# Performance work log

Measured on AMD Instinct MI355X. Metric: run time of the kernel, lower is better.

The kernel has to match this reference:

```python
import jax, jax.numpy as jnp
import numpy as np

D_MODEL = 1024
N_HEADS = 16
HEAD_DIM = D_MODEL // N_HEADS
SEQ_LEN = 2048
BATCH = 4


def setup_inputs() -> dict:
    key = jax.random.key(0)
    k1, k2, k3 = jax.random.split(key, 3)
    x = jax.random.normal(k1, (BATCH, SEQ_LEN, D_MODEL), dtype=jnp.float32)
    # Linear weights stored as [in, out] so y = x @ W (equivalent to torch x @ W.T)
    w_qkv = jax.random.normal(k2, (D_MODEL, 3 * D_MODEL), dtype=jnp.float32) * (D_MODEL ** -0.5)
    w_proj = jax.random.normal(k3, (D_MODEL, D_MODEL), dtype=jnp.float32) * (D_MODEL ** -0.5)
    return {"x": x, "w_qkv": w_qkv, "w_proj": w_proj}


def reference(x, w_qkv, w_proj):
    B, T, C = x.shape
    qkv = x @ w_qkv  # [B, T, 3C]
    q, k, v = jnp.split(qkv, 3, axis=-1)
    # [B, H, T, hd]
    q = q.reshape(B, T, N_HEADS, HEAD_DIM).transpose(0, 2, 1, 3)
    k = k.reshape(B, T, N_HEADS, HEAD_DIM).transpose(0, 2, 1, 3)
    v = v.reshape(B, T, N_HEADS, HEAD_DIM).transpose(0, 2, 1, 3)
    scale = HEAD_DIM ** -0.5
    attn = jnp.einsum("bhqd,bhkd->bhqk", q, k) * scale  # [B, H, T, T]
    causal = jnp.tril(jnp.ones((T, T), dtype=bool))
    attn = jnp.where(causal, attn, -jnp.inf)
    attn = jax.nn.softmax(attn, axis=-1)
    out = jnp.einsum("bhqk,bhkd->bhqd", attn, v)  # [B, H, T, hd]
    out = out.transpose(0, 2, 1, 3).reshape(B, T, C)
    return out @ w_proj
```

## Files before the change

### kernel.cpp

```cpp
#include <hip/hip_runtime.h>
#include <stdint.h>


typedef __bf16 bf16x8 __attribute__((ext_vector_type(8)));
typedef float f32x4 __attribute__((ext_vector_type(4)));
typedef unsigned short u16x8 __attribute__((ext_vector_type(8)));

#define DEVINL static __device__ __forceinline__

DEVINL unsigned short f2b(float f) {
  __bf16 h = (__bf16)f;
  return __builtin_bit_cast(unsigned short, h);
}

DEVINL void gld16(const void* g, void* l) {
  __builtin_amdgcn_global_load_lds(
      (const __attribute__((address_space(1))) void*)g,
      (__attribute__((address_space(3))) void*)l, 16, 0, 0);
}

DEVINL f32x4 mfma16(bf16x8 a, bf16x8 b, f32x4 c) {
  return __builtin_amdgcn_mfma_f32_16x16x32_bf16(a, b, c, 0, 0, 0);
}

#define SCHED_FENCE() __builtin_amdgcn_sched_barrier(0)

__global__ __launch_bounds__(256) void k_cast_bf16(const float* __restrict__ in,
                                                   unsigned short* __restrict__ out,
                                                   int n8) {
  int i = blockIdx.x * 256 + threadIdx.x;
  if (i >= n8) return;
  const float4* p = (const float4*)in + (size_t)i * 2;
  float4 a = p[0], b = p[1];
  u16x8 o;
  o[0] = f2b(a.x); o[1] = f2b(a.y); o[2] = f2b(a.z); o[3] = f2b(a.w);
  o[4] = f2b(b.x); o[5] = f2b(b.y); o[6] = f2b(b.z); o[7] = f2b(b.w);
  *(u16x8*)(out + (size_t)i * 8) = o;
}

__global__ __launch_bounds__(256) void k_transpose_w(const float* __restrict__ in,
                                                     unsigned short* __restrict__ out,
                                                     int R, int C) {
  __shared__ float t[64][65];
  int ci = blockIdx.x * 64, ri = blockIdx.y * 64;
  int tid = threadIdx.x;
#pragma unroll
  for (int j = 0; j < 4; ++j) {
    int c = tid + j * 256;
    int row = c >> 4;
    int col = (c & 15) * 4;
    float4 v = *(const float4*)(in + (size_t)(ri + row) * C + ci + col);
    t[row][col] = v.x; t[row][col + 1] = v.y; t[row][col + 2] = v.z; t[row][col + 3] = v.w;
  }
  __syncthreads();
  int cc = tid >> 2;
  int seg = (tid & 3) * 16;
  u16x8 o0, o1;
#pragma unroll
  for (int j = 0; j < 8; ++j) o0[j] = f2b(t[seg + j][cc]);
#pragma unroll
  for (int j = 0; j < 8; ++j) o1[j] = f2b(t[seg + 8 + j][cc]);
  unsigned short* dst = out + (size_t)(ci + cc) * R + ri + seg;
  *(u16x8*)dst = o0;
  *(u16x8*)(dst + 8) = o1;
}

template <int MODE>
__global__ __launch_bounds__(256) void k_gemm(const unsigned short* __restrict__ A,
                                              const unsigned short* __restrict__ Bt,
                                              int M, int N, int K,
                                              float* __restrict__ Cf,
                                              unsigned short* __restrict__ qo,
                                              unsigned short* __restrict__ ko,
                                              unsigned short* __restrict__ vo,
                                              float qscale) {
  __shared__ unsigned short As[3][128 * 32];
  __shared__ unsigned short Bs[3][128 * 32];
  int tid = threadIdx.x;
  int w = tid >> 6, lane = tid & 63, l15 = lane & 15, l4 = lane >> 4;
  int nwg = gridDim.x;
  int gx = N >> 7;
  int lin = blockIdx.x;
  int nx = nwg >> 3, rr = nwg & 7;
  int xcd = lin & 7, idx = lin >> 3;
  int wgid = (xcd < rr ? xcd * (nx + 1) : rr * (nx + 1) + (xcd - rr) * nx) + idx;
  int bn = wgid % gx, bm = wgid / gx;
  int wr = (w >> 1) * 64, wc = (w & 1) * 64;
  f32x4 acc[4][4];
#pragma unroll
  for (int i = 0; i < 4; ++i)
#pragma unroll
    for (int j = 0; j < 4; ++j) acc[i][j] = (f32x4){0.f, 0.f, 0.f, 0.f};
  const char* Ab = (const char*)(A + (size_t)bm * 128 * K);
  const char* Bb = (const char*)(Bt + (size_t)bn * 128 * K);
  int Lb0 = tid * 16, Lb1 = (tid + 256) * 16;
  int Nb0 = Lb0 ^ (((Lb0 >> 7) & 3) << 4);
  int Nb1 = Lb1 ^ (((Lb1 >> 7) & 3) << 4);
  int rA0 = Nb0 >> 6, o0 = Nb0 & 63;
  int rA1 = Nb1 >> 6, o1 = Nb1 & 63;

  auto stage = [&](int kt, int buf) {
    gld16(Ab + ((size_t)rA0 * K + kt) * 2 + o0, (char*)As[buf] + Lb0);
    gld16(Bb + ((size_t)rA0 * K + kt) * 2 + o0, (char*)Bs[buf] + Lb0);
    gld16(Ab + ((size_t)rA1 * K + kt) * 2 + o1, (char*)As[buf] + Lb1);
    gld16(Bb + ((size_t)rA1 * K + kt) * 2 + o1, (char*)Bs[buf] + Lb1);
  };

  const int nkt = K >> 5;
  stage(0, 0);
  stage(32, 1);
  SCHED_FENCE();
  for (int t = 0; t < nkt; ++t) {
    int cur = t - (t / 3) * 3;
    if (t) {
      SCHED_FENCE();
      __builtin_amdgcn_s_barrier();
      SCHED_FENCE();
    }
    if (t + 2 < nkt) {
      int nb = (t + 2) - ((t + 2) / 3) * 3;
      stage((t + 2) * 32, nb);
      SCHED_FENCE();
      asm volatile("s_waitcnt vmcnt(8)" ::: "memory");
    } else if (t + 1 < nkt) {
      SCHED_FENCE();
      asm volatile("s_waitcnt vmcnt(4)" ::: "memory");
    } else {
      SCHED_FENCE();
      asm volatile("s_waitcnt vmcnt(0)" ::: "memory");
    }
    SCHED_FENCE();
    __builtin_amdgcn_s_barrier();
    SCHED_FENCE();
    const char* Ac = (const char*)As[cur];
    const char* Bc = (const char*)Bs[cur];
    bf16x8 af[4], bfr[4];
#pragma unroll
    for (int m = 0; m < 4; ++m) {
      int nat = (wr + m * 16 + l15) * 64 + l4 * 16;
      af[m] = *(const bf16x8*)(Ac + (nat ^ (((nat >> 7) & 3) << 4)));
    }
#pragma unroll
    for (int n = 0; n < 4; ++n) {
      int nat = (wc + n * 16 + l15) * 64 + l4 * 16;
      bfr[n] = *(const bf16x8*)(Bc + (nat ^ (((nat >> 7) & 3) << 4)));
    }
    __builtin_amdgcn_s_setprio(1);
#pragma unroll
    for (int m = 0; m < 4; ++m)
#pragma unroll
      for (int n = 0; n < 4; ++n)
        acc[m][n] = mfma16(af[m], bfr[n], acc[m][n]);
    __builtin_amdgcn_s_setprio(0);
  }
#pragma unroll
  for (int m = 0; m < 4; ++m) {
    int grow0 = bm * 128 + wr + m * 16 + l4 * 4;
#pragma unroll
    for (int n = 0; n < 4; ++n) {
      int gcol = bn * 128 + wc + n * 16 + l15;
      if (MODE == 1) {
#pragma unroll
        for (int r = 0; r < 4; ++r)
          Cf[(size_t)(grow0 + r) * N + gcol] = acc[m][n][r];
      } else {
        int which = gcol >> 10, rem = gcol & 1023;
        int h = rem >> 6, d = rem & 63;
        int b = grow0 >> 11, t0 = grow0 & 2047;
        if (which == 2) {
          uint32_t lo = (uint32_t)f2b(acc[m][n][0]) | ((uint32_t)f2b(acc[m][n][1]) << 16);
          uint32_t hi = (uint32_t)f2b(acc[m][n][2]) | ((uint32_t)f2b(acc[m][n][3]) << 16);
          size_t off = (((size_t)(b * 16 + h)) * 64 + d) * 2048 + t0;
          *(uint2*)(vo + off) = make_uint2(lo, hi);
        } else {
          size_t off = (((size_t)(b * 16 + h)) * 2048 + t0) * 64 + d;
#pragma unroll
          for (int r = 0; r < 4; ++r) {
            float val = acc[m][n][r];
            if (which == 0) qo[off + (size_t)r * 64] = f2b(val * qscale);
            else            ko[off + (size_t)r * 64] = f2b(val);
          }
        }
      }
    }
  }
}

__global__ __launch_bounds__(512) void k_attn(const unsigned short* __restrict__ Q,
                                              const unsigned short* __restrict__ Kt,
                                              const unsigned short* __restrict__ Vt,
                                              unsigned short* __restrict__ AO) {
  __shared__ unsigned short Ks[2][4096];
  __shared__ unsigned short Vs[2][4096];
  __shared__ unsigned short Ps[8192];
  int tid = threadIdx.x;
  int w = tid >> 6, lane = tid & 63, l15 = lane & 15, l4 = lane >> 4;
  int lin = blockIdx.x;
  int xcd = lin & 7, jj = lin >> 3;
  int bh = xcd * 8 + (jj & 7);
  int p = jj >> 3;
  const char* Kb = (const char*)(Kt + (size_t)bh * 2048 * 64);
  const char* Vb = (const char*)(Vt + (size_t)bh * 64 * 2048);
  const int swp = (l15 & 7) << 4;
  char* Pw = (char*)Ps + w * 2048;
  int b = bh >> 4, h = bh & 15;

  int Lb0 = tid * 16;
  int Nb0 = Lb0 ^ (((Lb0 >> 7) & 7) << 4);
  int d0 = Nb0 >> 7, in0 = Nb0 & 127;

  auto stage = [&](int t, int buf) {
    size_t kv0 = (size_t)t * 64;
    gld16(Kb + kv0 * 128 + Nb0, (char*)Ks[buf] + Lb0);
    gld16(Vb + (size_t)d0 * 4096 + kv0 * 2 + in0, (char*)Vs[buf] + Lb0);
  };

  auto run = [&](int qi) {
    int q0 = qi * 128;
    const unsigned short* Qb = Q + ((size_t)bh * 2048 + q0 + w * 16) * 64;
    bf16x8 qf0 = *(const bf16x8*)((const char*)Qb + l15 * 128 + l4 * 16);
    bf16x8 qf1 = *(const bf16x8*)((const char*)Qb + l15 * 128 + 64 + l4 * 16);
    f32x4 o[4];
#pragma unroll
    for (int i = 0; i < 4; ++i) o[i] = (f32x4){0.f, 0.f, 0.f, 0.f};
    float mrow = -1e30f, lrow = 0.f;
    const int ntiles = 2 * qi + 2;
    const int qgmin = q0 + w * 16;
    const int qg = qgmin + l15;
    SCHED_FENCE();
    __builtin_amdgcn_s_barrier();
    SCHED_FENCE();
    stage(0, 0);
    SCHED_FENCE();
    for (int it = 0; it < ntiles; ++it) {
      int cur = it & 1;
      if (it) {
        SCHED_FENCE();
        __builtin_amdgcn_s_barrier();
        SCHED_FENCE();
      }
      if (it + 1 < ntiles) {
        stage(it + 1, cur ^ 1);
        SCHED_FENCE();
        asm volatile("s_waitcnt vmcnt(2)" ::: "memory");
      } else {
        SCHED_FENCE();
        asm volatile("s_waitcnt vmcnt(0)" ::: "memory");
      }
      SCHED_FENCE();
      __builtin_amdgcn_s_barrier();
      SCHED_FENCE();
      if (it * 64 <= qgmin + 15) {
        const char* Kc = (const char*)Ks[cur];
        const char* Vc = (const char*)Vs[cur];
        f32x4 s[4];
        __builtin_amdgcn_s_setprio(1);
#pragma unroll
        for (int c = 0; c < 4; ++c) {
          int row = c * 16 + l15;
          int base = row * 128 + l4 * 16;
          int sw = (row & 7) << 4;
          bf16x8 k0 = *(const bf16x8*)(Kc + (base ^ sw));
          bf16x8 k1 = *(const bf16x8*)(Kc + ((base + 64) ^ sw));
          f32x4 t = mfma16(k0, qf0, (f32x4){0.f, 0.f, 0.f, 0.f});
          s[c] = mfma16(k1, qf1, t);
        }
        __builtin_amdgcn_s_setprio(0);
        if (it * 64 + 63 > qgmin) {
#pragma unroll
          for (int c = 0; c < 4; ++c) {
            int kvb = it * 64 + c * 16 + l4 * 4;
#pragma unroll
            for (int r = 0; r < 4; ++r)
              if (kvb + r > qg) s[c][r] = -1e30f;
          }
        }
        float mx = fmaxf(fmaxf(fmaxf(s[0][0], s[0][1]), fmaxf(s[0][2], s[0][3])),
                         fmaxf(fmaxf(s[1][0], s[1][1]), fmaxf(s[1][2], s[1][3])));
        mx = fmaxf(mx, fmaxf(fmaxf(fmaxf(s[2][0], s[2][1]), fmaxf(s[2][2], s[2][3])),
                             fmaxf(fmaxf(s[3][0], s[3][1]), fmaxf(s[3][2], s[3][3]))));
        mx = fmaxf(mx, __shfl_xor(mx, 16));
        mx = fmaxf(mx, __shfl_xor(mx, 32));
        float mn = fmaxf(mrow, mx);
        float corr = __builtin_amdgcn_exp2f(mrow - mn);
        mrow = mn;
        float rs = 0.f;
#pragma unroll
        for (int c = 0; c < 4; ++c) {
          float p0 = __builtin_amdgcn_exp2f(s[c][0] - mn);
          float p1 = __builtin_amdgcn_exp2f(s[c][1] - mn);
          float p2 = __builtin_amdgcn_exp2f(s[c][2] - mn);
          float p3 = __builtin_amdgcn_exp2f(s[c][3] - mn);
          rs += (p0 + p1) + (p2 + p3);
          uint32_t lo = (uint32_t)f2b(p0) | ((uint32_t)f2b(p1) << 16);
          uint32_t hi = (uint32_t)f2b(p2) | ((uint32_t)f2b(p3) << 16);
          *(uint2*)(Pw + ((l15 * 128 + c * 32 + l4 * 8) ^ swp)) = make_uint2(lo, hi);
        }
        rs += __shfl_xor(rs, 16);
        rs += __shfl_xor(rs, 32);
        lrow = lrow * corr + rs;
        float corr_r[4];
#pragma unroll
        for (int r = 0; r < 4; ++r) corr_r[r] = __shfl(corr, l4 * 4 + r);
#pragma unroll
        for (int dc = 0; dc < 4; ++dc)
#pragma unroll
          for (int r = 0; r < 4; ++r) o[dc][r] *= corr_r[r];
        bf16x8 pa[2];
#pragma unroll
        for (int kc = 0; kc < 2; ++kc)
          pa[kc] = *(const bf16x8*)(Pw + ((l15 * 128 + kc * 64 + l4 * 16) ^ swp));
        __builtin_amdgcn_s_setprio(1);
#pragma unroll
        for (int dc = 0; dc < 4; ++dc) {
#pragma unroll
          for (int kc = 0; kc < 2; ++kc) {
            int vrow = dc * 16 + l15;
            int vnat = vrow * 128 + kc * 64 + l4 * 16;
            bf16x8 vb = *(const bf16x8*)(Vc + (vnat ^ ((vrow & 7) << 4)));
            o[dc] = mfma16(pa[kc], vb, o[dc]);
          }
        }
        __builtin_amdgcn_s_setprio(0);
      }
    }
    float inv[4];
#pragma unroll
    for (int r = 0; r < 4; ++r) inv[r] = 1.f / __shfl(lrow, l4 * 4 + r);
#pragma unroll
    for (int dc = 0; dc < 4; ++dc) {
#pragma unroll
      for (int r = 0; r < 4; ++r) {
        int t = q0 + w * 16 + l4 * 4 + r;
        AO[((size_t)(b * 2048 + t)) * 1024 + h * 64 + dc * 16 + l15] =
            f2b(o[dc][r] * inv[r]);
      }
    }
  };

  run(15 - p);
  run(p);
}

extern "C" void kernel_launch(void* const* d_in, const int* in_sizes, int n_in,
                              void* d_out, int out_size, void* d_ws, size_t ws_size,
                              hipStream_t stream) {
  const float* x      = (const float*)d_in[0];
  const float* w_qkv  = (const float*)d_in[1];
  const float* w_proj = (const float*)d_in[2];
  float* out = (float*)d_out;
  char* ws = (char*)d_ws;
  const size_t MB = 1024 * 1024;
  unsigned short* xb     = (unsigned short*)(ws);
  unsigned short* ao     = (unsigned short*)(ws);
  unsigned short* wqkvT  = (unsigned short*)(ws + 16 * MB);
  unsigned short* wprojT = (unsigned short*)(ws + 22 * MB);
  unsigned short* q      = (unsigned short*)(ws + 24 * MB);
  unsigned short* k      = (unsigned short*)(ws + 40 * MB);
  unsigned short* vT     = (unsigned short*)(ws + 56 * MB);

  k_cast_bf16<<<4096, 256, 0, stream>>>(x, xb, 1048576);
  k_transpose_w<<<dim3(48, 16), 256, 0, stream>>>(w_qkv, wqkvT, 1024, 3072);
  k_transpose_w<<<dim3(16, 16), 256, 0, stream>>>(w_proj, wprojT, 1024, 1024);
  const float qscale = 0.125f * 1.44269504088896f;
  k_gemm<0><<<1536, 256, 0, stream>>>(xb, wqkvT, 8192, 3072, 1024,
                                      nullptr, q, k, vT, qscale);
  k_attn<<<512, 512, 0, stream>>>(q, k, vT, ao);
  k_gemm<1><<<512, 256, 0, stream>>>(ao, wprojT, 8192, 1024, 1024,
                                     out, nullptr, nullptr, nullptr, 1.f);
}
```

Measured before the change: 183.1 us.

## Software-pipeline QK^T one tile ahead of softmax and PV in attention

```diff
diff --git a/kernel.cpp b/kernel.cpp
--- a/kernel.cpp
+++ b/kernel.cpp
@@ -209,10 +209,11 @@
   int Nb0 = Lb0 ^ (((Lb0 >> 7) & 7) << 4);
   int d0 = Nb0 >> 7, in0 = Nb0 & 127;
 
-  auto stage = [&](int t, int buf) {
-    size_t kv0 = (size_t)t * 64;
-    gld16(Kb + kv0 * 128 + Nb0, (char*)Ks[buf] + Lb0);
-    gld16(Vb + (size_t)d0 * 4096 + kv0 * 2 + in0, (char*)Vs[buf] + Lb0);
+  auto stageK = [&](int t, int buf) {
+    gld16(Kb + (size_t)t * 8192 + Nb0, (char*)Ks[buf] + Lb0);
+  };
+  auto stageV = [&](int t, int buf) {
+    gld16(Vb + (size_t)d0 * 4096 + (size_t)t * 128 + in0, (char*)Vs[buf] + Lb0);
   };
 
   auto run = [&](int qi) {
@@ -227,58 +228,72 @@
     const int ntiles = 2 * qi + 2;
     const int qgmin = q0 + w * 16;
     const int qg = qgmin + l15;
+
+    auto computeQK = [&](f32x4 (&s)[4], int tau) {
+      const char* Kc = (const char*)Ks[tau & 1];
+      __builtin_amdgcn_s_setprio(1);
+#pragma unroll
+      for (int c = 0; c < 4; ++c) {
+        int row = c * 16 + l15;
+        int base = row * 128 + l4 * 16;
+        int sw = (row & 7) << 4;
+        bf16x8 k0 = *(const bf16x8*)(Kc + (base ^ sw));
+        bf16x8 k1 = *(const bf16x8*)(Kc + ((base + 64) ^ sw));
+        f32x4 t = mfma16(k0, qf0, (f32x4){0.f, 0.f, 0.f, 0.f});
+        s[c] = mfma16(k1, qf1, t);
+      }
+      __builtin_amdgcn_s_setprio(0);
+      if (tau * 64 + 63 > qgmin) {
+#pragma unroll
+        for (int c = 0; c < 4; ++c) {
+          int kvb = tau * 64 + c * 16 + l4 * 4;
+#pragma unroll
+          for (int r = 0; r < 4; ++r)
+            if (kvb + r > qg) s[c][r] = -1e30f;
+        }
+      }
+    };
+
     SCHED_FENCE();
     __builtin_amdgcn_s_barrier();
     SCHED_FENCE();
-    stage(0, 0);
-    SCHED_FENCE();
-    for (int it = 0; it < ntiles; ++it) {
-      int cur = it & 1;
-      if (it) {
-        SCHED_FENCE();
-        __builtin_amdgcn_s_barrier();
-        SCHED_FENCE();
-      }
-      if (it + 1 < ntiles) {
-        stage(it + 1, cur ^ 1);
-        SCHED_FENCE();
+    stageK(0, 0);
+    stageV(0, 0);
+    stageK(1, 1);
+    SCHED_FENCE();
+    asm volatile("s_waitcnt vmcnt(2)" ::: "memory");
+    SCHED_FENCE();
+    __builtin_amdgcn_s_barrier();
+    SCHED_FENCE();
+    f32x4 sp[4];
+    computeQK(sp, 0);
+
+    for (int t = 0; t < ntiles; ++t) {
+      SCHED_FENCE();
+      __builtin_amdgcn_s_barrier();
+      SCHED_FENCE();
+      if (t + 2 < ntiles) stageK(t + 2, t & 1);
+      if (t + 1 < ntiles) stageV(t + 1, (t + 1) & 1);
+      SCHED_FENCE();
+      if (t + 2 < ntiles) {
         asm volatile("s_waitcnt vmcnt(2)" ::: "memory");
+      } else if (t + 1 < ntiles) {
+        asm volatile("s_waitcnt vmcnt(1)" ::: "memory");
       } else {
-        SCHED_FENCE();
         asm volatile("s_waitcnt vmcnt(0)" ::: "memory");
       }
       SCHED_FENCE();
       __builtin_amdgcn_s_barrier();
       SCHED_FENCE();
-      if (it * 64 <= qgmin + 15) {
-        const char* Kc = (const char*)Ks[cur];
-        const char* Vc = (const char*)Vs[cur];
-        f32x4 s[4];
-        __builtin_amdgcn_s_setprio(1);
-#pragma unroll
-        for (int c = 0; c < 4; ++c) {
-          int row = c * 16 + l15;
-          int base = row * 128 + l4 * 16;
-          int sw = (row & 7) << 4;
-          bf16x8 k0 = *(const bf16x8*)(Kc + (base ^ sw));
-          bf16x8 k1 = *(const bf16x8*)(Kc + ((base + 64) ^ sw));
-          f32x4 t = mfma16(k0, qf0, (f32x4){0.f, 0.f, 0.f, 0.f});
-          s[c] = mfma16(k1, qf1, t);
-        }
-        __builtin_amdgcn_s_setprio(0);
-        if (it * 64 + 63 > qgmin) {
-#pragma unroll
-          for (int c = 0; c < 4; ++c) {
-            int kvb = it * 64 + c * 16 + l4 * 4;
-#pragma unroll
-            for (int r = 0; r < 4; ++r)
-              if (kvb + r > qg) s[c][r] = -1e30f;
-          }
-        }
-        float mx = fmaxf(fmaxf(fmaxf(s[0][0], s[0][1]), fmaxf(s[0][2], s[0][3])),
-                         fmaxf(fmaxf(s[1][0], s[1][1]), fmaxf(s[1][2], s[1][3])));
-        mx = fmaxf(mx, fmaxf(fmaxf(fmaxf(s[2][0], s[2][1]), fmaxf(s[2][2], s[2][3])),
-                             fmaxf(fmaxf(s[3][0], s[3][1]), fmaxf(s[3][2], s[3][3]))));
+      f32x4 sc[4];
+      bool doQK = (t + 1 < ntiles) && ((t + 1) * 64 <= qgmin + 15);
+      if (doQK) computeQK(sc, t + 1);
+      if (t * 64 <= qgmin + 15) {
+        const char* Vc = (const char*)Vs[t & 1];
+        float mx = fmaxf(fmaxf(fmaxf(sp[0][0], sp[0][1]), fmaxf(sp[0][2], sp[0][3])),
+                         fmaxf(fmaxf(sp[1][0], sp[1][1]), fmaxf(sp[1][2], sp[1][3])));
+        mx = fmaxf(mx, fmaxf(fmaxf(fmaxf(sp[2][0], sp[2][1]), fmaxf(sp[2][2], sp[2][3])),
+                             fmaxf(fmaxf(sp[3][0], sp[3][1]), fmaxf(sp[3][2], sp[3][3]))));
         mx = fmaxf(mx, __shfl_xor(mx, 16));
         mx = fmaxf(mx, __shfl_xor(mx, 32));
         float mn = fmaxf(mrow, mx);
@@ -287,10 +302,10 @@
         float rs = 0.f;
 #pragma unroll
         for (int c = 0; c < 4; ++c) {
-          float p0 = __builtin_amdgcn_exp2f(s[c][0] - mn);
-          float p1 = __builtin_amdgcn_exp2f(s[c][1] - mn);
-          float p2 = __builtin_amdgcn_exp2f(s[c][2] - mn);
-          float p3 = __builtin_amdgcn_exp2f(s[c][3] - mn);
+          float p0 = __builtin_amdgcn_exp2f(sp[c][0] - mn);
+          float p1 = __builtin_amdgcn_exp2f(sp[c][1] - mn);
+          float p2 = __builtin_amdgcn_exp2f(sp[c][2] - mn);
+          float p3 = __builtin_amdgcn_exp2f(sp[c][3] - mn);
           rs += (p0 + p1) + (p2 + p3);
           uint32_t lo = (uint32_t)f2b(p0) | ((uint32_t)f2b(p1) << 16);
           uint32_t hi = (uint32_t)f2b(p2) | ((uint32_t)f2b(p3) << 16);
@@ -323,6 +338,8 @@
         }
         __builtin_amdgcn_s_setprio(0);
       }
+#pragma unroll
+      for (int c = 0; c < 4; ++c) sp[c] = sc[c];
     }
     float inv[4];
 #pragma unroll
```

After: 185.5 us. Within noise of the previous version (+1.3%).
